# Optimization experiments

Hardware: AMD Instinct MI355X
Metric: run time of the kernel (lower is better)

## Reference

```python
import jax, jax.numpy as jnp
import numpy as np

NUM_HEADS = 16

def setup_inputs() -> dict:
    key = jax.random.key(0)
    k1, k2, k3 = jax.random.split(key, 3)
    B, N, C = 2, 2048, 256
    hidden = 4 * C  # 1024
    head_dim = hidden // NUM_HEADS  # 64
    array = jax.random.normal(k1, (B, N, C), dtype=jnp.float32)
    Wqkv = jax.random.normal(k2, (C, 3 * hidden), dtype=jnp.float32) * 0.02
    # Original code projects to q.shape[-1] == head_dim (quirk preserved)
    Wout = jax.random.normal(k3, (hidden, head_dim), dtype=jnp.float32) * 0.02
    return {"array": array, "Wqkv": Wqkv, "Wout": Wout}

def reference(array, Wqkv, Wout):
    B, N, C = array.shape
    H = NUM_HEADS
    qkv = array @ Wqkv                      # (B, N, 3*hidden)
    q, k, v = jnp.split(qkv, 3, axis=-1)    # each (B, N, hidden)
    def to_heads(a):
        return a.reshape(B, N, H, -1).transpose(0, 2, 1, 3)  # (B, H, N, d)
    q, k, v = map(to_heads, (q, k, v))
    d = q.shape[-1]
    scores = jnp.einsum('bhid,bhjd->bhij', q, k) / jnp.sqrt(jnp.float32(d))
    attn = jax.nn.softmax(scores, axis=-1)   # dropout is deterministic no-op
    out = jnp.einsum('bhij,bhjd->bhid', attn, v)
    out = out.transpose(0, 2, 1, 3).reshape(B, N, H * d)  # (B, N, hidden)
    return out @ Wout                        # (B, N, head_dim)
```

## Files before the change

kernel.cpp:

```cpp
#include <hip/hip_runtime.h>
#include <hip/hip_bf16.h>
#include <math.h>

typedef __attribute__((ext_vector_type(8))) short bf16x8;
typedef __attribute__((ext_vector_type(4))) float f32x4;
typedef __attribute__((ext_vector_type(4))) unsigned u32x4;
typedef __attribute__((ext_vector_type(2))) unsigned u32x2;

union bfpack { u32x4 u; bf16x8 h; };

__device__ inline unsigned bfraw(float f) {
    union { float f; unsigned u; } x; x.f = f;
    return x.u + 0x8000u;
}
__device__ inline short f2bf(float f) { return (short)(bfraw(f) >> 16); }
__device__ inline unsigned pkbf(float lo, float hi) {
    return __builtin_amdgcn_perm(bfraw(hi), bfraw(lo), 0x07060302);
}
__device__ inline float fast_exp2(float x) {
#if __has_builtin(__builtin_amdgcn_exp2f)
    return __builtin_amdgcn_exp2f(x);
#else
    return exp2f(x);
#endif
}
__device__ inline void gl_lds16(const short* g, short* l) {
    __builtin_amdgcn_global_load_lds(
        (const __attribute__((address_space(1))) unsigned*)g,
        (__attribute__((address_space(3))) unsigned*)l, 16, 0, 0);
}
#define SCQ 0.18033688011112042f

__global__ __launch_bounds__(256) void trans_kernel(
        const float* __restrict__ src, short* __restrict__ dst, int R, int C) {
    __shared__ float T[64][65];
    int r0 = blockIdx.y * 64, c0 = blockIdx.x * 64;
    int t = threadIdx.x;
    {
        int kr = t >> 2, ns = (t & 3) * 16;
        const float* s = src + (size_t)(r0 + kr) * C + c0 + ns;
#pragma unroll
        for (int j = 0; j < 4; ++j) {
            f32x4 v = *(const f32x4*)(s + j * 4);
#pragma unroll
            for (int e = 0; e < 4; ++e) T[kr][ns + j * 4 + e] = v[e];
        }
    }
    __syncthreads();
    {
        int n = t >> 2, ks = (t & 3) * 16;
        bfpack p0, p1;
#pragma unroll
        for (int j = 0; j < 4; ++j) {
            float a = T[ks + 2 * j][n], b = T[ks + 2 * j + 1][n];
            p0.u[j] = pkbf(a, b);
        }
#pragma unroll
        for (int j = 0; j < 4; ++j) {
            float a = T[ks + 8 + 2 * j][n], b = T[ks + 8 + 2 * j + 1][n];
            p1.u[j] = pkbf(a, b);
        }
        short* d = dst + (size_t)(c0 + n) * R + r0 + ks;
        *(bf16x8*)d = p0.h;
        *(bf16x8*)(d + 8) = p1.h;
    }
}

__global__ __launch_bounds__(256) void qkv_kernel(
        const float* __restrict__ A, const short* __restrict__ Wt,
        short* __restrict__ Qb, short* __restrict__ Kb, short* __restrict__ Vt) {
    __shared__ short As[128 * 64];
    __shared__ short Bs[128 * 64];
    int m0 = blockIdx.x * 128;
    int n0 = blockIdx.y * 128;
    int t = threadIdx.x;
    int wave = t >> 6, lane = t & 63;
    int quad = lane >> 4, l16 = lane & 15;
    int r8 = lane >> 3, c8 = lane & 7;
    f32x4 acc[2][8] = {};
    for (int it = 0; it < 4; ++it) {
        int k0 = it * 64;
        __syncthreads();
#pragma unroll
        for (int j = 0; j < 4; ++j) {
            int row = wave * 32 + j * 8 + r8;
            int clog = c8 ^ (row & 7);
            gl_lds16(Wt + (size_t)(n0 + row) * 256 + k0 + clog * 8,
                     &Bs[(wave * 32 + j * 8) * 64]);
        }
        {
            int row = t >> 1, half = t & 1;
            const float* as = A + (size_t)(m0 + row) * 256 + k0 + half * 32;
#pragma unroll
            for (int cc = 0; cc < 2; ++cc) {
                f32x4 a0 = ((const f32x4*)as)[cc * 4 + 0];
                f32x4 a1 = ((const f32x4*)as)[cc * 4 + 1];
                f32x4 a2 = ((const f32x4*)as)[cc * 4 + 2];
                f32x4 a3 = ((const f32x4*)as)[cc * 4 + 3];
                bfpack v0, v1;
                v0.u[0] = pkbf(a0[0], a0[1]); v0.u[1] = pkbf(a0[2], a0[3]);
                v0.u[2] = pkbf(a1[0], a1[1]); v0.u[3] = pkbf(a1[2], a1[3]);
                v1.u[0] = pkbf(a2[0], a2[1]); v1.u[1] = pkbf(a2[2], a2[3]);
                v1.u[2] = pkbf(a3[0], a3[1]); v1.u[3] = pkbf(a3[2], a3[3]);
                int cl0 = half * 4 + cc * 2;
                *(bf16x8*)&As[row * 64 + ((cl0    ) ^ (row & 7)) * 8] = v0.h;
                *(bf16x8*)&As[row * 64 + ((cl0 + 1) ^ (row & 7)) * 8] = v1.h;
            }
        }
        __syncthreads();
        bf16x8 af[2][2];
#pragma unroll
        for (int s = 0; s < 2; ++s) {
            int m = wave * 32 + s * 16 + l16;
#pragma unroll
            for (int kh = 0; kh < 2; ++kh)
                af[s][kh] = *(const bf16x8*)&As[m * 64 + (((quad + 4 * kh)) ^ (m & 7)) * 8];
        }
#pragma unroll
        for (int c = 0; c < 8; ++c) {
            int n = c * 16 + l16;
            bf16x8 b0 = *(const bf16x8*)&Bs[n * 64 + ((quad    ) ^ (n & 7)) * 8];
            bf16x8 b1 = *(const bf16x8*)&Bs[n * 64 + ((quad + 4) ^ (n & 7)) * 8];
#pragma unroll
            for (int s = 0; s < 2; ++s) {
                acc[s][c] = __builtin_amdgcn_mfma_f32_16x16x32_bf16(af[s][0], b0, acc[s][c], 0, 0, 0);
                acc[s][c] = __builtin_amdgcn_mfma_f32_16x16x32_bf16(af[s][1], b1, acc[s][c], 0, 0, 0);
            }
        }
    }
    int sel = n0 >> 10;
    int b = m0 >> 11;
    int nb = (m0 & 2047) + wave * 32;
#pragma unroll
    for (int s = 0; s < 2; ++s) {
#pragma unroll
        for (int c = 0; c < 8; ++c) {
            int gc = n0 + c * 16 + l16;
            int h = (gc >> 6) & 15, dim = gc & 63;
            int n_base = nb + s * 16 + quad * 4;
            if (sel == 2) {
                u32x2 pk;
                pk[0] = pkbf(acc[s][c][0], acc[s][c][1]);
                pk[1] = pkbf(acc[s][c][2], acc[s][c][3]);
                *(u32x2*)&Vt[(((size_t)(b * 16 + h) * 64 + dim) << 11) + n_base] = pk;
            } else {
                short* dst = (sel == 0) ? Qb : Kb;
                float sc = (sel == 0) ? SCQ : 1.0f;
#pragma unroll
                for (int r = 0; r < 4; ++r)
                    dst[(((size_t)(b * 16 + h) * 2048 + n_base + r) << 6) + dim] =
                        f2bf(acc[s][c][r] * sc);
            }
        }
    }
}

__global__ __launch_bounds__(256, 2) void attn_kernel(
        const short* __restrict__ Qb, const short* __restrict__ Kb,
        const short* __restrict__ Vt, short* __restrict__ AO) {
    __shared__ short KT[2][64 * 64];
    __shared__ short VT[2][64 * 64];
    int bh = blockIdx.y, qt = blockIdx.x;
    int b = bh >> 4, h = bh & 15;
    int t = threadIdx.x, wave = t >> 6, lane = t & 63;
    int quad = lane >> 4, l16 = lane & 15;
    const short* Qp = Qb + (size_t)bh * (2048 * 64);
    const short* Kp = Kb + (size_t)bh * (2048 * 64);
    const short* Vp = Vt + (size_t)bh * (64 * 2048);
    int q0 = qt * 128 + wave * 32;

    bf16x8 qf[2][2];
#pragma unroll
    for (int sq = 0; sq < 2; ++sq) {
        const short* qp = Qp + (size_t)(q0 + sq * 16 + l16) * 64 + quad * 8;
        qf[sq][0] = *(const bf16x8*)qp;
        qf[sq][1] = *(const bf16x8*)(qp + 32);
    }
    int r8 = lane >> 3, p8 = lane & 7;
    int kr0 = wave * 16 + r8, kr1 = kr0 + 8;
    int swz0 = (kr0 & 3) | (((kr0 >> 3) & 1) << 2);
    int swz1 = (kr1 & 3) | (((kr1 >> 3) & 1) << 2);
    const short* gk0 = Kp + kr0 * 64 + (p8 ^ swz0) * 8;
    const short* gk1 = Kp + kr1 * 64 + (p8 ^ swz1) * 8;
    const short* gv0 = Vp + kr0 * 2048 + (p8 ^ (kr0 & 7)) * 8;
    const short* gv1 = Vp + kr1 * 2048 + (p8 ^ (kr1 & 7)) * 8;
    int ldsk0 = wave * 1024, ldsk1 = wave * 1024 + 512;
    int swzk = (l16 & 3) | (((l16 >> 2) & 1) << 2);
    int krd = ((l16 >> 2) * 8 + (l16 & 3)) * 64;
    int koff0 = krd + ((quad ^ swzk) * 8);
    int koff1 = krd + (((quad + 4) ^ swzk) * 8);
    int voff0 = l16 * 64 + ((quad ^ (l16 & 7)) * 8);
    int voff1 = l16 * 64 + (((quad + 4) ^ (l16 & 7)) * 8);

    f32x4 o[2][4] = {};
    f32x4 ol[2] = {};
    bf16x8 ones = {(short)0x3F80, (short)0x3F80, (short)0x3F80, (short)0x3F80,
                   (short)0x3F80, (short)0x3F80, (short)0x3F80, (short)0x3F80};

    gl_lds16(gk0, &KT[0][ldsk0]);
    gl_lds16(gk1, &KT[0][ldsk1]);
    gl_lds16(gv0, &VT[0][ldsk0]);
    gl_lds16(gv1, &VT[0][ldsk1]);

    for (int kt = 0; kt < 32; ++kt) {
        __syncthreads();
        if (kt + 1 < 32) {
            int buf = (kt + 1) & 1;
            gl_lds16(gk0 + (size_t)(kt + 1) * 4096, &KT[buf][ldsk0]);
            gl_lds16(gk1 + (size_t)(kt + 1) * 4096, &KT[buf][ldsk1]);
            gl_lds16(gv0 + (kt + 1) * 64, &VT[buf][ldsk0]);
            gl_lds16(gv1 + (kt + 1) * 64, &VT[buf][ldsk1]);
        }
        const short* kb = &KT[kt & 1][0];
        const short* vb = &VT[kt & 1][0];
        bf16x8 kc[8], vc[8];
#pragma unroll
        for (int hh = 0; hh < 2; ++hh)
#pragma unroll
            for (int ab = 0; ab < 2; ++ab) {
                kc[(hh * 2 + ab) * 2 + 0] = *(const bf16x8*)&kb[koff0 + ab * 256 + hh * 2048];
                kc[(hh * 2 + ab) * 2 + 1] = *(const bf16x8*)&kb[koff1 + ab * 256 + hh * 2048];
            }
#pragma unroll
        for (int hh = 0; hh < 2; ++hh)
#pragma unroll
            for (int dt = 0; dt < 4; ++dt)
                vc[hh * 4 + dt] = *(const bf16x8*)&vb[(hh ? voff1 : voff0) + dt * 1024];

#pragma unroll
        for (int sq = 0; sq < 2; ++sq) {
            f32x4 s[4];
#pragma unroll
            for (int i = 0; i < 4; ++i) {
                f32x4 z = {};
                z = __builtin_amdgcn_mfma_f32_16x16x32_bf16(kc[2 * i], qf[sq][0], z, 0, 0, 0);
                z = __builtin_amdgcn_mfma_f32_16x16x32_bf16(kc[2 * i + 1], qf[sq][1], z, 0, 0, 0);
                s[i] = z;
            }
            bfpack pa0, pa1;
#pragma unroll
            for (int ab = 0; ab < 2; ++ab) {
                float p0 = fast_exp2(s[ab][0]),      p1 = fast_exp2(s[ab][1]);
                float p2 = fast_exp2(s[ab][2]),      p3 = fast_exp2(s[ab][3]);
                float q0e = fast_exp2(s[2 + ab][0]), q1e = fast_exp2(s[2 + ab][1]);
                float q2e = fast_exp2(s[2 + ab][2]), q3e = fast_exp2(s[2 + ab][3]);
                pa0.u[ab * 2 + 0] = pkbf(p0, p1);
                pa0.u[ab * 2 + 1] = pkbf(p2, p3);
                pa1.u[ab * 2 + 0] = pkbf(q0e, q1e);
                pa1.u[ab * 2 + 1] = pkbf(q2e, q3e);
            }
            ol[sq] = __builtin_amdgcn_mfma_f32_16x16x32_bf16(pa0.h, ones, ol[sq], 0, 0, 0);
            ol[sq] = __builtin_amdgcn_mfma_f32_16x16x32_bf16(pa1.h, ones, ol[sq], 0, 0, 0);
#pragma unroll
            for (int dt = 0; dt < 4; ++dt) {
                o[sq][dt] = __builtin_amdgcn_mfma_f32_16x16x32_bf16(pa0.h, vc[dt],
                                                                    o[sq][dt], 0, 0, 0);
                o[sq][dt] = __builtin_amdgcn_mfma_f32_16x16x32_bf16(pa1.h, vc[4 + dt],
                                                                    o[sq][dt], 0, 0, 0);
            }
        }
    }
#pragma unroll
    for (int sq = 0; sq < 2; ++sq) {
        f32x4 inv;
#pragma unroll
        for (int r = 0; r < 4; ++r) inv[r] = 1.0f / ol[sq][r];
#pragma unroll
        for (int dt = 0; dt < 4; ++dt)
#pragma unroll
            for (int r = 0; r < 4; ++r) {
                int qrow = q0 + sq * 16 + quad * 4 + r;
                AO[((size_t)(b * 2048 + qrow)) * 1024 + h * 64 + dt * 16 + l16] =
                    f2bf(o[sq][dt][r] * inv[r]);
            }
    }
}

__global__ __launch_bounds__(256) void out_kernel(
        const short* __restrict__ AO, const short* __restrict__ Wo,
        float* __restrict__ Out) {
    __shared__ short As[64 * 64];
    __shared__ short Bs[64 * 64];
    int m0 = blockIdx.x * 64;
    int t = threadIdx.x, wave = t >> 6, lane = t & 63;
    int quad = lane >> 4, l16 = lane & 15;
    int r8 = lane >> 3, c8 = lane & 7;
    f32x4 acc[4] = {};
    for (int it = 0; it < 16; ++it) {
        int k0 = it * 64;
        __syncthreads();
#pragma unroll
        for (int j = 0; j < 2; ++j) {
            int row = wave * 16 + j * 8 + r8;
            int clog = c8 ^ (row & 7);
            gl_lds16(AO + (size_t)(m0 + row) * 1024 + k0 + clog * 8,
                     &As[(wave * 16 + j * 8) * 64]);
            gl_lds16(Wo + (size_t)row * 1024 + k0 + clog * 8,
                     &Bs[(wave * 16 + j * 8) * 64]);
        }
        __syncthreads();
        int m = wave * 16 + l16;
        bf16x8 a0 = *(const bf16x8*)&As[m * 64 + ((quad    ) ^ (m & 7)) * 8];
        bf16x8 a1 = *(const bf16x8*)&As[m * 64 + ((quad + 4) ^ (m & 7)) * 8];
#pragma unroll
        for (int c = 0; c < 4; ++c) {
            int n = c * 16 + l16;
            bf16x8 b0 = *(const bf16x8*)&Bs[n * 64 + ((quad    ) ^ (n & 7)) * 8];
            bf16x8 b1 = *(const bf16x8*)&Bs[n * 64 + ((quad + 4) ^ (n & 7)) * 8];
            acc[c] = __builtin_amdgcn_mfma_f32_16x16x32_bf16(a0, b0, acc[c], 0, 0, 0);
            acc[c] = __builtin_amdgcn_mfma_f32_16x16x32_bf16(a1, b1, acc[c], 0, 0, 0);
        }
    }
#pragma unroll
    for (int c = 0; c < 4; ++c)
#pragma unroll
        for (int r = 0; r < 4; ++r) {
            int gm = m0 + wave * 16 + quad * 4 + r;
            Out[((size_t)gm << 6) + c * 16 + l16] = acc[c][r];
        }
}

extern "C" void kernel_launch(void* const* d_in, const int* in_sizes, int n_in,
                              void* d_out, int out_size, void* d_ws, size_t ws_size,
                              hipStream_t stream) {
    const float* A    = (const float*)d_in[0];
    const float* Wqkv = (const float*)d_in[1];
    const float* Wout = (const float*)d_in[2];
    float* Out = (float*)d_out;

    short* ws = (short*)d_ws;
    short* Wq = ws;
    short* Wo = ws + 786432;
    short* Qb = ws + 851968;
    short* Kb = ws + 5046272;
    short* Vt = ws + 9240576;
    short* AO = ws + 13434880;

    hipLaunchKernelGGL(trans_kernel, dim3(48, 4), dim3(256), 0, stream, Wqkv, Wq, 256, 3072);
    hipLaunchKernelGGL(trans_kernel, dim3(1, 16), dim3(256), 0, stream, Wout, Wo, 1024, 64);
    hipLaunchKernelGGL(qkv_kernel, dim3(32, 24), dim3(256), 0, stream, A, Wq, Qb, Kb, Vt);
    hipLaunchKernelGGL(attn_kernel, dim3(16, 32), dim3(256), 0, stream, Qb, Kb, Vt, AO);
    hipLaunchKernelGGL(out_kernel, dim3(64), dim3(256), 0, stream, AO, Wo, Out);
}
```

Before: 138.4 us.

## Fuse output projection into attention kernel with atomic accumulation, halve query tile

Removes the separate output-projection kernel and the bf16 attention-output buffer. Each attention block now multiplies its normalized per-head output tile by that head's slice of Wout through LDS and MFMA, then atomically adds fp32 partials into the output, which a new zero kernel clears first. The query tile per wave drops from 32 to 16 rows, doubling the grid and raising the occupancy hint to 4 blocks. The cost is 16-way float atomic contention per output element, nondeterministic summation order, and double the K/V tile loads per query.

```diff
diff --git a/kernel.cpp b/kernel.cpp
--- a/kernel.cpp
+++ b/kernel.cpp
@@ -30,6 +30,12 @@
         (__attribute__((address_space(3))) unsigned*)l, 16, 0, 0);
 }
 #define SCQ 0.18033688011112042f
+
+__global__ __launch_bounds__(256) void zero_kernel(float* __restrict__ p) {
+    int i = blockIdx.x * 256 + threadIdx.x;
+    f32x4 z = {};
+    ((f32x4*)p)[i] = z;
+}
 
 __global__ __launch_bounds__(256) void trans_kernel(
         const float* __restrict__ src, short* __restrict__ dst, int R, int C) {
@@ -51,15 +57,9 @@
         int n = t >> 2, ks = (t & 3) * 16;
         bfpack p0, p1;
 #pragma unroll
-        for (int j = 0; j < 4; ++j) {
-            float a = T[ks + 2 * j][n], b = T[ks + 2 * j + 1][n];
-            p0.u[j] = pkbf(a, b);
-        }
-#pragma unroll
-        for (int j = 0; j < 4; ++j) {
-            float a = T[ks + 8 + 2 * j][n], b = T[ks + 8 + 2 * j + 1][n];
-            p1.u[j] = pkbf(a, b);
-        }
+        for (int j = 0; j < 4; ++j) p0.u[j] = pkbf(T[ks + 2 * j][n], T[ks + 2 * j + 1][n]);
+#pragma unroll
+        for (int j = 0; j < 4; ++j) p1.u[j] = pkbf(T[ks + 8 + 2 * j][n], T[ks + 9 + 2 * j][n]);
         short* d = dst + (size_t)(c0 + n) * R + r0 + ks;
         *(bf16x8*)d = p0.h;
         *(bf16x8*)(d + 8) = p1.h;
@@ -155,9 +155,10 @@
     }
 }
 
-__global__ __launch_bounds__(256, 2) void attn_kernel(
+__global__ __launch_bounds__(256, 4) void attn_kernel(
         const short* __restrict__ Qb, const short* __restrict__ Kb,
-        const short* __restrict__ Vt, short* __restrict__ AO) {
+        const short* __restrict__ Vt, const short* __restrict__ Wo,
+        float* __restrict__ Out) {
     __shared__ short KT[2][64 * 64];
     __shared__ short VT[2][64 * 64];
     int bh = blockIdx.y, qt = blockIdx.x;
@@ -167,14 +168,13 @@
     const short* Qp = Qb + (size_t)bh * (2048 * 64);
     const short* Kp = Kb + (size_t)bh * (2048 * 64);
     const short* Vp = Vt + (size_t)bh * (64 * 2048);
-    int q0 = qt * 128 + wave * 32;
-
-    bf16x8 qf[2][2];
-#pragma unroll
-    for (int sq = 0; sq < 2; ++sq) {
-        const short* qp = Qp + (size_t)(q0 + sq * 16 + l16) * 64 + quad * 8;
-        qf[sq][0] = *(const bf16x8*)qp;
-        qf[sq][1] = *(const bf16x8*)(qp + 32);
+    int q0 = qt * 64 + wave * 16;
+
+    bf16x8 qf0, qf1;
+    {
+        const short* qp = Qp + (size_t)(q0 + l16) * 64 + quad * 8;
+        qf0 = *(const bf16x8*)qp;
+        qf1 = *(const bf16x8*)(qp + 32);
     }
     int r8 = lane >> 3, p8 = lane & 7;
     int kr0 = wave * 16 + r8, kr1 = kr0 + 8;
@@ -192,8 +192,8 @@
     int voff0 = l16 * 64 + ((quad ^ (l16 & 7)) * 8);
     int voff1 = l16 * 64 + (((quad + 4) ^ (l16 & 7)) * 8);
 
-    f32x4 o[2][4] = {};
-    f32x4 ol[2] = {};
+    f32x4 o[4] = {};
+    f32x4 ol = {};
     bf16x8 ones = {(short)0x3F80, (short)0x3F80, (short)0x3F80, (short)0x3F80,
                    (short)0x3F80, (short)0x3F80, (short)0x3F80, (short)0x3F80};
 
@@ -227,97 +227,72 @@
             for (int dt = 0; dt < 4; ++dt)
                 vc[hh * 4 + dt] = *(const bf16x8*)&vb[(hh ? voff1 : voff0) + dt * 1024];
 
-#pragma unroll
-        for (int sq = 0; sq < 2; ++sq) {
-            f32x4 s[4];
-#pragma unroll
-            for (int i = 0; i < 4; ++i) {
-                f32x4 z = {};
-                z = __builtin_amdgcn_mfma_f32_16x16x32_bf16(kc[2 * i], qf[sq][0], z, 0, 0, 0);
-                z = __builtin_amdgcn_mfma_f32_16x16x32_bf16(kc[2 * i + 1], qf[sq][1], z, 0, 0, 0);
-                s[i] = z;
-            }
-            bfpack pa0, pa1;
-#pragma unroll
-            for (int ab = 0; ab < 2; ++ab) {
-                float p0 = fast_exp2(s[ab][0]),      p1 = fast_exp2(s[ab][1]);
-                float p2 = fast_exp2(s[ab][2]),      p3 = fast_exp2(s[ab][3]);
-                float q0e = fast_exp2(s[2 + ab][0]), q1e = fast_exp2(s[2 + ab][1]);
-                float q2e = fast_exp2(s[2 + ab][2]), q3e = fast_exp2(s[2 + ab][3]);
-                pa0.u[ab * 2 + 0] = pkbf(p0, p1);
-                pa0.u[ab * 2 + 1] = pkbf(p2, p3);
-                pa1.u[ab * 2 + 0] = pkbf(q0e, q1e);
-                pa1.u[ab * 2 + 1] = pkbf(q2e, q3e);
-            }
-            ol[sq] = __builtin_amdgcn_mfma_f32_16x16x32_bf16(pa0.h, ones, ol[sq], 0, 0, 0);
-            ol[sq] = __builtin_amdgcn_mfma_f32_16x16x32_bf16(pa1.h, ones, ol[sq], 0, 0, 0);
-#pragma unroll
-            for (int dt = 0; dt < 4; ++dt) {
-                o[sq][dt] = __builtin_amdgcn_mfma_f32_16x16x32_bf16(pa0.h, vc[dt],
-                                                                    o[sq][dt], 0, 0, 0);
-                o[sq][dt] = __builtin_amdgcn_mfma_f32_16x16x32_bf16(pa1.h, vc[4 + dt],
-                                                                    o[sq][dt], 0, 0, 0);
-            }
-        }
-    }
-#pragma unroll
-    for (int sq = 0; sq < 2; ++sq) {
-        f32x4 inv;
-#pragma unroll
-        for (int r = 0; r < 4; ++r) inv[r] = 1.0f / ol[sq][r];
-#pragma unroll
-        for (int dt = 0; dt < 4; ++dt)
-#pragma unroll
-            for (int r = 0; r < 4; ++r) {
-                int qrow = q0 + sq * 16 + quad * 4 + r;
-                AO[((size_t)(b * 2048 + qrow)) * 1024 + h * 64 + dt * 16 + l16] =
-                    f2bf(o[sq][dt][r] * inv[r]);
-            }
-    }
-}
-
-__global__ __launch_bounds__(256) void out_kernel(
-        const short* __restrict__ AO, const short* __restrict__ Wo,
-        float* __restrict__ Out) {
-    __shared__ short As[64 * 64];
-    __shared__ short Bs[64 * 64];
-    int m0 = blockIdx.x * 64;
-    int t = threadIdx.x, wave = t >> 6, lane = t & 63;
-    int quad = lane >> 4, l16 = lane & 15;
-    int r8 = lane >> 3, c8 = lane & 7;
-    f32x4 acc[4] = {};
-    for (int it = 0; it < 16; ++it) {
-        int k0 = it * 64;
-        __syncthreads();
-#pragma unroll
-        for (int j = 0; j < 2; ++j) {
-            int row = wave * 16 + j * 8 + r8;
-            int clog = c8 ^ (row & 7);
-            gl_lds16(AO + (size_t)(m0 + row) * 1024 + k0 + clog * 8,
-                     &As[(wave * 16 + j * 8) * 64]);
-            gl_lds16(Wo + (size_t)row * 1024 + k0 + clog * 8,
-                     &Bs[(wave * 16 + j * 8) * 64]);
-        }
-        __syncthreads();
-        int m = wave * 16 + l16;
-        bf16x8 a0 = *(const bf16x8*)&As[m * 64 + ((quad    ) ^ (m & 7)) * 8];
-        bf16x8 a1 = *(const bf16x8*)&As[m * 64 + ((quad + 4) ^ (m & 7)) * 8];
-#pragma unroll
-        for (int c = 0; c < 4; ++c) {
-            int n = c * 16 + l16;
-            bf16x8 b0 = *(const bf16x8*)&Bs[n * 64 + ((quad    ) ^ (n & 7)) * 8];
-            bf16x8 b1 = *(const bf16x8*)&Bs[n * 64 + ((quad + 4) ^ (n & 7)) * 8];
-            acc[c] = __builtin_amdgcn_mfma_f32_16x16x32_bf16(a0, b0, acc[c], 0, 0, 0);
-            acc[c] = __builtin_amdgcn_mfma_f32_16x16x32_bf16(a1, b1, acc[c], 0, 0, 0);
-        }
-    }
-#pragma unroll
-    for (int c = 0; c < 4; ++c)
+        f32x4 s[4];
+#pragma unroll
+        for (int i = 0; i < 4; ++i) {
+            f32x4 z = {};
+            z = __builtin_amdgcn_mfma_f32_16x16x32_bf16(kc[2 * i], qf0, z, 0, 0, 0);
+            z = __builtin_amdgcn_mfma_f32_16x16x32_bf16(kc[2 * i + 1], qf1, z, 0, 0, 0);
+            s[i] = z;
+        }
+        bfpack pa0, pa1;
+#pragma unroll
+        for (int ab = 0; ab < 2; ++ab) {
+            float p0 = fast_exp2(s[ab][0]),      p1 = fast_exp2(s[ab][1]);
+            float p2 = fast_exp2(s[ab][2]),      p3 = fast_exp2(s[ab][3]);
+            float q0e = fast_exp2(s[2 + ab][0]), q1e = fast_exp2(s[2 + ab][1]);
+            float q2e = fast_exp2(s[2 + ab][2]), q3e = fast_exp2(s[2 + ab][3]);
+            pa0.u[ab * 2 + 0] = pkbf(p0, p1);
+            pa0.u[ab * 2 + 1] = pkbf(p2, p3);
+            pa1.u[ab * 2 + 0] = pkbf(q0e, q1e);
+            pa1.u[ab * 2 + 1] = pkbf(q2e, q3e);
+        }
+        ol = __builtin_amdgcn_mfma_f32_16x16x32_bf16(pa0.h, ones, ol, 0, 0, 0);
+        ol = __builtin_amdgcn_mfma_f32_16x16x32_bf16(pa1.h, ones, ol, 0, 0, 0);
+#pragma unroll
+        for (int dt = 0; dt < 4; ++dt) {
+            o[dt] = __builtin_amdgcn_mfma_f32_16x16x32_bf16(pa0.h, vc[dt],     o[dt], 0, 0, 0);
+            o[dt] = __builtin_amdgcn_mfma_f32_16x16x32_bf16(pa1.h, vc[4 + dt], o[dt], 0, 0, 0);
+        }
+    }
+
+    short* WsL = &KT[0][0];
+    short* myO = &VT[0][wave * 1024];
+#pragma unroll
+    for (int j = 0; j < 2; ++j) {
+        int n = wave * 16 + j * 8 + r8;
+        gl_lds16(Wo + (size_t)n * 1024 + h * 64 + ((p8 ^ (n & 7)) * 8),
+                 &WsL[(wave * 16 + j * 8) * 64]);
+    }
+    f32x4 inv;
+#pragma unroll
+    for (int r = 0; r < 4; ++r) inv[r] = 1.0f / ol[r];
+#pragma unroll
+    for (int dt = 0; dt < 4; ++dt) {
 #pragma unroll
         for (int r = 0; r < 4; ++r) {
-            int gm = m0 + wave * 16 + quad * 4 + r;
-            Out[((size_t)gm << 6) + c * 16 + l16] = acc[c][r];
-        }
+            int q = quad * 4 + r;
+            int col = dt * 16 + l16;
+            int c = col >> 3;
+            myO[q * 64 + ((c ^ (q & 7)) * 8) + (col & 7)] = f2bf(o[dt][r] * inv[r]);
+        }
+    }
+    __syncthreads();
+    bf16x8 a0 = *(const bf16x8*)&myO[l16 * 64 + ((quad       ^ (l16 & 7)) * 8)];
+    bf16x8 a1 = *(const bf16x8*)&myO[l16 * 64 + (((quad + 4) ^ (l16 & 7)) * 8)];
+    float* OutRow = Out + ((size_t)(b * 2048 + q0)) * 64;
+#pragma unroll
+    for (int c = 0; c < 4; ++c) {
+        int n = c * 16 + l16;
+        bf16x8 b0 = *(const bf16x8*)&WsL[n * 64 + ((quad       ^ (n & 7)) * 8)];
+        bf16x8 b1 = *(const bf16x8*)&WsL[n * 64 + (((quad + 4) ^ (n & 7)) * 8)];
+        f32x4 rg = {};
+        rg = __builtin_amdgcn_mfma_f32_16x16x32_bf16(a0, b0, rg, 0, 0, 0);
+        rg = __builtin_amdgcn_mfma_f32_16x16x32_bf16(a1, b1, rg, 0, 0, 0);
+#pragma unroll
+        for (int r = 0; r < 4; ++r)
+            atomicAdd(&OutRow[(quad * 4 + r) * 64 + n], rg[r]);
+    }
 }
 
 extern "C" void kernel_launch(void* const* d_in, const int* in_sizes, int n_in,
@@ -334,11 +309,10 @@
     short* Qb = ws + 851968;
     short* Kb = ws + 5046272;
     short* Vt = ws + 9240576;
-    short* AO = ws + 13434880;
-
+
+    hipLaunchKernelGGL(zero_kernel, dim3(256), dim3(256), 0, stream, Out);
     hipLaunchKernelGGL(trans_kernel, dim3(48, 4), dim3(256), 0, stream, Wqkv, Wq, 256, 3072);
     hipLaunchKernelGGL(trans_kernel, dim3(1, 16), dim3(256), 0, stream, Wout, Wo, 1024, 64);
     hipLaunchKernelGGL(qkv_kernel, dim3(32, 24), dim3(256), 0, stream, A, Wq, Qb, Kb, Vt);
-    hipLaunchKernelGGL(attn_kernel, dim3(16, 32), dim3(256), 0, stream, Qb, Kb, Vt, AO);
-    hipLaunchKernelGGL(out_kernel, dim3(64), dim3(256), 0, stream, AO, Wo, Out);
-}
+    hipLaunchKernelGGL(attn_kernel, dim3(32, 32), dim3(256), 0, stream, Qb, Kb, Vt, Wo, Out);
+}
```

Measured after the change: 137.7 us. Within noise of the previous version (-0.5%).
